# Performance work log

Hardware: AMD Instinct MI355X
Metric: run time of the kernel (lower is better)

The kernel has to match this reference:

```python
import jax, jax.numpy as jnp
import numpy as np

B, NF, EC, H, W = 16, 64, 3, 256, 256
NF1, NF2 = NF // 8, NF // 4  # 8, 16

def _leaky(x):
    return jnp.where(x >= 0, x, 0.2 * x)

def setup_inputs() -> dict:
    key = jax.random.key(0)
    ks = jax.random.split(key, 10)
    s = lambda fan_in: 1.0 / np.sqrt(fan_in)
    return {
        "feature_maps": jax.random.normal(ks[0], (B, NF, H, W), dtype=jnp.float32),
        "extra_maps": jax.random.normal(ks[1], (B, EC, H, W), dtype=jnp.float32),
        "w1": jax.random.uniform(ks[2], (NF1, EC), jnp.float32, -s(EC), s(EC)),
        "b1": jax.random.uniform(ks[3], (NF1,), jnp.float32, -s(EC), s(EC)),
        "w2": jax.random.uniform(ks[4], (NF2, NF1), jnp.float32, -s(NF1), s(NF1)),
        "b2": jax.random.uniform(ks[5], (NF2,), jnp.float32, -s(NF1), s(NF1)),
        "wm": jax.random.uniform(ks[6], (NF, NF2), jnp.float32, -s(NF2), s(NF2)),
        "bm": jax.random.uniform(ks[7], (NF,), jnp.float32, -s(NF2), s(NF2)),
        "wa": jax.random.uniform(ks[8], (NF, NF2), jnp.float32, -s(NF2), s(NF2)),
        "ba": jax.random.uniform(ks[9], (NF,), jnp.float32, -s(NF2), s(NF2)),
    }

def reference(feature_maps, extra_maps, w1, b1, w2, b2, wm, bm, wa, ba):
    # 1x1 convs expressed as channel contractions (per-pixel MLP chain)
    fea1 = _leaky(jnp.einsum('oc,bchw->bohw', w1, extra_maps) + b1[:, None, None])
    fea2 = _leaky(jnp.einsum('oc,bchw->bohw', w2, fea1) + b2[:, None, None])
    mul = jnp.einsum('oc,bchw->bohw', wm, fea2) + bm[:, None, None]
    add = jnp.einsum('oc,bchw->bohw', wa, fea2) + ba[:, None, None]
    # out = add / (1 + feature_maps * mul)
    return add / (1.0 + feature_maps * mul)
```

## Files before the change

### kernel.cpp

```cpp
#include <hip/hip_runtime.h>

#define HW 65536
#define NPIX (16 * HW)
#define PX 2
#define THREADS 256

#define OFF_W1 0
#define OFF_B1 24
#define OFF_W2 32
#define OFF_B2 160
#define OFF_WM 176
#define OFF_BM 1200
#define OFF_WA 1264
#define OFF_BA 2288
#define NWTOT  2352

__device__ __forceinline__ double leakyd(double x) {
    return fmax(x, 0.2 * x);
}

__global__ __launch_bounds__(THREADS) void attcnn_kernel(
    const float* __restrict__ fm,
    const float* __restrict__ ex,
    const float* __restrict__ w1,
    const float* __restrict__ b1,
    const float* __restrict__ w2,
    const float* __restrict__ b2,
    const float* __restrict__ wm,
    const float* __restrict__ bm,
    const float* __restrict__ wa,
    const float* __restrict__ ba,
    float* __restrict__ out)
{
    __shared__ double sd[NWTOT];

    const int tid = threadIdx.x;
    if (tid < 24)  sd[OFF_W1 + tid] = (double)w1[tid];
    if (tid < 8)   sd[OFF_B1 + tid] = (double)b1[tid];
    if (tid < 128) sd[OFF_W2 + tid] = (double)w2[tid];
    if (tid < 16)  sd[OFF_B2 + tid] = (double)b2[tid];
    if (tid < 64)  { sd[OFF_BM + tid] = (double)bm[tid];
                     sd[OFF_BA + tid] = (double)ba[tid]; }
    #pragma unroll
    for (int i = 0; i < 4; ++i) {
        sd[OFF_WM + tid + i * 256] = (double)wm[tid + i * 256];
        sd[OFF_WA + tid + i * 256] = (double)wa[tid + i * 256];
    }
    __syncthreads();

    const long base = ((long)blockIdx.x * THREADS + tid) * PX;
    const int b  = (int)(base >> 16);
    const int hw = (int)(base & 65535);

    const float* exp_ = ex + (long)b * 3 * HW + hw;
    const float2 e0 = *(const float2*)(exp_);
    const float2 e1 = *(const float2*)(exp_ + HW);
    const float2 e2 = *(const float2*)(exp_ + 2 * HW);
    const double e0d[2] = {(double)e0.x, (double)e0.y};
    const double e1d[2] = {(double)e1.x, (double)e1.y};
    const double e2d[2] = {(double)e2.x, (double)e2.y};

    double f1[8][2];
    #pragma unroll
    for (int j = 0; j < 8; ++j) {
        const double c0 = sd[OFF_W1 + j * 3 + 0];
        const double c1 = sd[OFF_W1 + j * 3 + 1];
        const double c2 = sd[OFF_W1 + j * 3 + 2];
        const double bb = sd[OFF_B1 + j];
        #pragma unroll
        for (int p = 0; p < 2; ++p)
            f1[j][p] = leakyd(fma(c0, e0d[p], fma(c1, e1d[p], fma(c2, e2d[p], bb))));
    }

    double f2[16][2];
    #pragma unroll
    for (int k = 0; k < 16; ++k) {
        double a0 = sd[OFF_B2 + k], a1 = a0;
        #pragma unroll
        for (int j = 0; j < 8; ++j) {
            const double w = sd[OFF_W2 + k * 8 + j];
            a0 = fma(w, f1[j][0], a0);
            a1 = fma(w, f1[j][1], a1);
        }
        f2[k][0] = leakyd(a0);
        f2[k][1] = leakyd(a1);
    }

    const float* fmp = fm  + (long)b * 64 * HW + hw;
    float*       op  = out + (long)b * 64 * HW + hw;

    #pragma unroll 2
    for (int o = 0; o < 64; ++o) {
        double m0 = sd[OFF_BM + o], m1 = m0;
        double a0 = sd[OFF_BA + o], a1 = a0;
        #pragma unroll
        for (int k = 0; k < 16; ++k) {
            const double wmv = sd[OFF_WM + o * 16 + k];
            const double wav = sd[OFF_WA + o * 16 + k];
            m0 = fma(wmv, f2[k][0], m0);
            m1 = fma(wmv, f2[k][1], m1);
            a0 = fma(wav, f2[k][0], a0);
            a1 = fma(wav, f2[k][1], a1);
        }
        const float2 f = *(const float2*)(fmp + (long)o * HW);
        const double den0 = fma((double)f.x, m0, 1.0);
        const double den1 = fma((double)f.y, m1, 1.0);
        float h0 = (float)den0;
        float h1 = (float)den1;
        float r0 = __builtin_amdgcn_rcpf(h0);
        float r1 = __builtin_amdgcn_rcpf(h1);
        r0 = r0 * fmaf(-h0, r0, 2.0f);
        r1 = r1 * fmaf(-h1, r1, 2.0f);
        float2 o2;
        o2.x = (float)a0 * r0;
        o2.y = (float)a1 * r1;
        *(float2*)(op + (long)o * HW) = o2;
    }
}

extern "C" void kernel_launch(void* const* d_in, const int* in_sizes, int n_in,
                              void* d_out, int out_size, void* d_ws, size_t ws_size,
                              hipStream_t stream) {
    const float* fm = (const float*)d_in[0];
    const float* ex = (const float*)d_in[1];
    const float* w1 = (const float*)d_in[2];
    const float* b1 = (const float*)d_in[3];
    const float* w2 = (const float*)d_in[4];
    const float* b2 = (const float*)d_in[5];
    const float* wm = (const float*)d_in[6];
    const float* bm = (const float*)d_in[7];
    const float* wa = (const float*)d_in[8];
    const float* ba = (const float*)d_in[9];
    float* out = (float*)d_out;

    const int total_threads = NPIX / PX;
    const int blocks = total_threads / THREADS;
    attcnn_kernel<<<blocks, THREADS, 0, stream>>>(fm, ex, w1, b1, w2, b2,
                                                  wm, bm, wa, ba, out);
}
```

Measured before the change: 473.6 us.

## Use one pixel per thread, fp32 add branch, and prefetch feature maps in chunks

Each thread now handles one pixel instead of two and is launched with a launch-bounds occupancy hint. The `add` projection moves from fp64 to fp32, while the `mul` path stays in fp64 because the denominator is sensitive. Feature-map loads are software-pipelined in chunks of eight channels to hide memory latency. The aim is to cut fp64 FMA throughput cost and raise occupancy, at the price of slightly lower precision on the add path and more threads each doing the shared weight loads.

```diff
diff --git a/kernel.cpp b/kernel.cpp
--- a/kernel.cpp
+++ b/kernel.cpp
@@ -2,24 +2,14 @@
 
 #define HW 65536
 #define NPIX (16 * HW)
-#define PX 2
 #define THREADS 256
 
-#define OFF_W1 0
-#define OFF_B1 24
-#define OFF_W2 32
-#define OFF_B2 160
-#define OFF_WM 176
-#define OFF_BM 1200
-#define OFF_WA 1264
-#define OFF_BA 2288
-#define NWTOT  2352
 
 __device__ __forceinline__ double leakyd(double x) {
     return fmax(x, 0.2 * x);
 }
 
-__global__ __launch_bounds__(THREADS) void attcnn_kernel(
+__global__ __launch_bounds__(THREADS, 4) void attcnn_kernel(
     const float* __restrict__ fm,
     const float* __restrict__ ex,
     const float* __restrict__ w1,
@@ -32,89 +22,93 @@
     const float* __restrict__ ba,
     float* __restrict__ out)
 {
-    __shared__ double sd[NWTOT];
+    __shared__ double s_w1[24];
+    __shared__ double s_b1[8];
+    __shared__ double s_w2[128];
+    __shared__ double s_b2[16];
+    __shared__ double s_wm[1024];
+    __shared__ double s_bm[64];
+    __shared__ float  s_wa[1024];
+    __shared__ float  s_ba[64];
 
     const int tid = threadIdx.x;
-    if (tid < 24)  sd[OFF_W1 + tid] = (double)w1[tid];
-    if (tid < 8)   sd[OFF_B1 + tid] = (double)b1[tid];
-    if (tid < 128) sd[OFF_W2 + tid] = (double)w2[tid];
-    if (tid < 16)  sd[OFF_B2 + tid] = (double)b2[tid];
-    if (tid < 64)  { sd[OFF_BM + tid] = (double)bm[tid];
-                     sd[OFF_BA + tid] = (double)ba[tid]; }
+    if (tid < 24)  s_w1[tid] = (double)w1[tid];
+    if (tid < 8)   s_b1[tid] = (double)b1[tid];
+    if (tid < 128) s_w2[tid] = (double)w2[tid];
+    if (tid < 16)  s_b2[tid] = (double)b2[tid];
+    if (tid < 64)  { s_bm[tid] = (double)bm[tid]; s_ba[tid] = ba[tid]; }
     #pragma unroll
     for (int i = 0; i < 4; ++i) {
-        sd[OFF_WM + tid + i * 256] = (double)wm[tid + i * 256];
-        sd[OFF_WA + tid + i * 256] = (double)wa[tid + i * 256];
+        s_wm[tid + i * 256] = (double)wm[tid + i * 256];
+        s_wa[tid + i * 256] = wa[tid + i * 256];
     }
     __syncthreads();
 
-    const long base = ((long)blockIdx.x * THREADS + tid) * PX;
-    const int b  = (int)(base >> 16);
-    const int hw = (int)(base & 65535);
+    const int idx = blockIdx.x * THREADS + tid;
+    const int b   = idx >> 16;
+    const int hw  = idx & 65535;
 
     const float* exp_ = ex + (long)b * 3 * HW + hw;
-    const float2 e0 = *(const float2*)(exp_);
-    const float2 e1 = *(const float2*)(exp_ + HW);
-    const float2 e2 = *(const float2*)(exp_ + 2 * HW);
-    const double e0d[2] = {(double)e0.x, (double)e0.y};
-    const double e1d[2] = {(double)e1.x, (double)e1.y};
-    const double e2d[2] = {(double)e2.x, (double)e2.y};
+    const double e0 = (double)exp_[0];
+    const double e1 = (double)exp_[HW];
+    const double e2 = (double)exp_[2 * HW];
 
-    double f1[8][2];
+    double f1v[8];
     #pragma unroll
     for (int j = 0; j < 8; ++j) {
-        const double c0 = sd[OFF_W1 + j * 3 + 0];
-        const double c1 = sd[OFF_W1 + j * 3 + 1];
-        const double c2 = sd[OFF_W1 + j * 3 + 2];
-        const double bb = sd[OFF_B1 + j];
-        #pragma unroll
-        for (int p = 0; p < 2; ++p)
-            f1[j][p] = leakyd(fma(c0, e0d[p], fma(c1, e1d[p], fma(c2, e2d[p], bb))));
+        f1v[j] = leakyd(fma(s_w1[j * 3 + 0], e0,
+                        fma(s_w1[j * 3 + 1], e1,
+                        fma(s_w1[j * 3 + 2], e2, s_b1[j]))));
     }
 
-    double f2[16][2];
+    double f2d[16];
+    float  f2s[16];
     #pragma unroll
     for (int k = 0; k < 16; ++k) {
-        double a0 = sd[OFF_B2 + k], a1 = a0;
+        double acc = s_b2[k];
         #pragma unroll
-        for (int j = 0; j < 8; ++j) {
-            const double w = sd[OFF_W2 + k * 8 + j];
-            a0 = fma(w, f1[j][0], a0);
-            a1 = fma(w, f1[j][1], a1);
-        }
-        f2[k][0] = leakyd(a0);
-        f2[k][1] = leakyd(a1);
+        for (int j = 0; j < 8; ++j)
+            acc = fma(s_w2[k * 8 + j], f1v[j], acc);
+        acc = leakyd(acc);
+        f2d[k] = acc;
+        f2s[k] = (float)acc;
     }
 
     const float* fmp = fm  + (long)b * 64 * HW + hw;
     float*       op  = out + (long)b * 64 * HW + hw;
 
-    #pragma unroll 2
-    for (int o = 0; o < 64; ++o) {
-        double m0 = sd[OFF_BM + o], m1 = m0;
-        double a0 = sd[OFF_BA + o], a1 = a0;
+    float fcur[8], fnxt[8];
+    #pragma unroll
+    for (int i = 0; i < 8; ++i) fcur[i] = fmp[(long)i * HW];
+
+    #pragma unroll 1
+    for (int c = 0; c < 8; ++c) {
+        const int ob = c * 8;
+        if (c < 7) {
+            #pragma unroll
+            for (int i = 0; i < 8; ++i)
+                fnxt[i] = fmp[(long)(ob + 8 + i) * HW];
+        }
         #pragma unroll
-        for (int k = 0; k < 16; ++k) {
-            const double wmv = sd[OFF_WM + o * 16 + k];
-            const double wav = sd[OFF_WA + o * 16 + k];
-            m0 = fma(wmv, f2[k][0], m0);
-            m1 = fma(wmv, f2[k][1], m1);
-            a0 = fma(wav, f2[k][0], a0);
-            a1 = fma(wav, f2[k][1], a1);
+        for (int i = 0; i < 8; ++i) {
+            const int o = ob + i;
+            double m = s_bm[o];
+            float  a = s_ba[o];
+            #pragma unroll
+            for (int k = 0; k < 16; ++k) {
+                m = fma(s_wm[o * 16 + k], f2d[k], m);
+                a = fmaf(s_wa[o * 16 + k], f2s[k], a);
+            }
+            const double den = fma((double)fcur[i], m, 1.0);
+            float h = (float)den;
+            float r = __builtin_amdgcn_rcpf(h);
+            r = r * fmaf(-h, r, 2.0f);
+            op[(long)o * HW] = a * r;
         }
-        const float2 f = *(const float2*)(fmp + (long)o * HW);
-        const double den0 = fma((double)f.x, m0, 1.0);
-        const double den1 = fma((double)f.y, m1, 1.0);
-        float h0 = (float)den0;
-        float h1 = (float)den1;
-        float r0 = __builtin_amdgcn_rcpf(h0);
-        float r1 = __builtin_amdgcn_rcpf(h1);
-        r0 = r0 * fmaf(-h0, r0, 2.0f);
-        r1 = r1 * fmaf(-h1, r1, 2.0f);
-        float2 o2;
-        o2.x = (float)a0 * r0;
-        o2.y = (float)a1 * r1;
-        *(float2*)(op + (long)o * HW) = o2;
+        if (c < 7) {
+            #pragma unroll
+            for (int i = 0; i < 8; ++i) fcur[i] = fnxt[i];
+        }
     }
 }
 
@@ -133,8 +127,7 @@
     const float* ba = (const float*)d_in[9];
     float* out = (float*)d_out;
 
-    const int total_threads = NPIX / PX;
-    const int blocks = total_threads / THREADS;
+    const int blocks = NPIX / THREADS;
     attcnn_kernel<<<blocks, THREADS, 0, stream>>>(fm, ex, w1, b1, w2, b2,
                                                   wm, bm, wa, ba, out);
 }
```

Measured after the change: 473.3 us. No clear change (-0.1%).
